# Performance work log

Measured on AMD Instinct MI355X. Metric: run time of the kernel, lower is better.

Reference implementation:

```python
import jax, jax.numpy as jnp
import numpy as np

N, D = 4096, 512
NUM_CLASSES = 100


def setup_inputs() -> dict:
    key = jax.random.key(0)
    k1, k2, k3 = jax.random.split(key, 3)
    image_features = jax.random.normal(k1, (N, D), dtype=jnp.float32)
    text_features = jax.random.normal(k2, (N, D), dtype=jnp.float32)
    labels = jax.random.randint(k3, (N,), 0, NUM_CLASSES, dtype=jnp.int64)
    return {
        "image_features": image_features,
        "text_features": text_features,
        "labels": labels,
    }


def reference(image_features, text_features, labels):
    # mask[i,j] = 1 if labels[i] != labels[j] else 0 (vectorized O(N^2) loops)
    mask = (labels[:, None] != labels[None, :]).astype(image_features.dtype)  # [N,N]

    # L2-normalize along feature dim (F.normalize, p=2, dim=1)
    img = image_features / jnp.linalg.norm(image_features, axis=1, keepdims=True)
    txt = text_features / jnp.linalg.norm(text_features, axis=1, keepdims=True)

    # neg_similarity = sum(exp((txt @ img.T) @ mask))  -- faithful to source
    sim = txt @ img.T                      # [N,N]
    neg_similarity = jnp.sum(jnp.exp(sim @ mask))

    # pos_sim_i = exp(<img_i, txt_i>); loss_i = log(pos / (pos + neg))
    pos_sim = jnp.exp(jnp.sum(img * txt, axis=1))  # [N]
    pos_log = jnp.log(pos_sim / (pos_sim + neg_similarity))
    return -jnp.sum(pos_log)
```

## Files before the change

kernel.cpp:

```cpp
#include <hip/hip_runtime.h>

#define NN 4096
#define DD 512
#define CP 128
#define MT 16
#define NBB 256
#define LROWS 64

#define NEG   0
#define DONE  1
#define D_OFF 16
#define CNTF_OFF (16 + NN)
#define GB_OFF_W (16 + NN + CP)

typedef __attribute__((ext_vector_type(8))) short bf16x8;
typedef __attribute__((ext_vector_type(4))) float f32x4;

static __device__ inline unsigned short f2bf(float f) {
    unsigned int u = __float_as_uint(f);
    unsigned int r = u + 0x7fffu + ((u >> 16) & 1u);
    return (unsigned short)(r >> 16);
}

__global__ __launch_bounds__(512, 1) void kA(const float* __restrict__ img,
                                             const int* __restrict__ labels,
                                             float* __restrict__ ws) {
    __shared__ __align__(16) float lrows[LROWS * DD];
    __shared__ int   wlist[8][32];
    __shared__ int   wcnt[8];
    __shared__ int   soff[9];
    __shared__ int   flat[256];
    __shared__ float sinv[256];
    int c = blockIdx.x, t = threadIdx.x, w = t >> 6, l = t & 63;

    if (c == 0 && t == 0) { ws[NEG] = 0.0f; ((int*)ws)[DONE] = 0; }

    int cnt = 0;
    for (int it = 0; it < 8; ++it) {
        int row = (w << 9) + (it << 6) + l;
        int lab = labels[row];
        unsigned long long m = __ballot(lab == c);
        if (lab == c) {
            int pos = cnt + (int)__popcll(m & ((1ull << l) - 1ull));
            if (pos < 32) wlist[w][pos] = row;
        }
        cnt += (int)__popcll(m);
    }
    if (l == 0) wcnt[w] = cnt < 32 ? cnt : 32;
    __syncthreads();
    if (t == 0) {
        int o = 0;
        #pragma unroll
        for (int i = 0; i < 8; ++i) { soff[i] = o; o += wcnt[i]; }
        soff[8] = o;
    }
    __syncthreads();
    int n = soff[8];
    for (int s = l; s < wcnt[w]; s += 64) flat[soff[w] + s] = wlist[w][s];
    __syncthreads();

    int nl = n < LROWS ? n : LROWS;
    const float4* img4 = (const float4*)img;
    float4* lr4 = (float4*)lrows;

    for (int idx = t; idx < nl * 128; idx += 512) {
        int r = idx >> 7, c4 = idx & 127;
        lr4[r * 128 + c4] = img4[(size_t)flat[r] * 128 + c4];
    }
    __syncthreads();

    for (int s = w; s < n; s += 8) {
        float4 v0, v1;
        if (s < nl) { v0 = lr4[s * 128 + l]; v1 = lr4[s * 128 + 64 + l]; }
        else { int j = flat[s]; v0 = img4[(size_t)j * 128 + l]; v1 = img4[(size_t)j * 128 + 64 + l]; }
        float ss = v0.x*v0.x + v0.y*v0.y + v0.z*v0.z + v0.w*v0.w
                 + v1.x*v1.x + v1.y*v1.y + v1.z*v1.z + v1.w*v1.w;
        #pragma unroll
        for (int o = 32; o >= 1; o >>= 1) ss += __shfl_xor(ss, o);
        if (l == 0) sinv[s] = rsqrtf(ss);
    }
    __syncthreads();

    float acc = 0.f;
    #pragma unroll 8
    for (int s = 0; s < nl; ++s) acc += lrows[s * DD + t] * sinv[s];
    for (int s = nl; s < n; ++s) acc += img[(size_t)flat[s] * DD + t] * sinv[s];

    unsigned short* gbf = (unsigned short*)(ws + GB_OFF_W);
    gbf[(size_t)c * DD + t] = f2bf(acc);
    if (t == 0) ws[CNTF_OFF + c] = (float)n;
}

__global__ __launch_bounds__(256, 1) void kB(const float* __restrict__ img,
                                             const float* __restrict__ txt,
                                             float* __restrict__ ws,
                                             float* __restrict__ out) {
    __shared__ __align__(16) unsigned char As[MT * 1024];
    __shared__ __align__(16) unsigned char Bs[CP * 1024];
    __shared__ float cnts[CP];
    __shared__ float part[4][MT];
    __shared__ float Ss[MT];
    __shared__ float wred[4];
    __shared__ float sneg;
    __shared__ int   sdone;

    int t = threadIdx.x, w = t >> 6, l = t & 63;
    int b = blockIdx.x;
    int row0 = b * MT;
    int* wsi = (int*)ws;

    #pragma unroll
    for (int i = 0; i < 4; ++i) {
        int lr  = w * 4 + i;
        int row = row0 + lr;
        const float4* i4 = (const float4*)(img + (size_t)row * DD);
        const float4* t4 = (const float4*)(txt + (size_t)row * DD);
        float4 a0 = i4[l], a1 = i4[l + 64];
        float4 b0 = t4[l], b1 = t4[l + 64];
        float ssi = a0.x*a0.x + a0.y*a0.y + a0.z*a0.z + a0.w*a0.w
                  + a1.x*a1.x + a1.y*a1.y + a1.z*a1.z + a1.w*a1.w;
        float sst = b0.x*b0.x + b0.y*b0.y + b0.z*b0.z + b0.w*b0.w
                  + b1.x*b1.x + b1.y*b1.y + b1.z*b1.z + b1.w*b1.w;
        float dot = a0.x*b0.x + a0.y*b0.y + a0.z*b0.z + a0.w*b0.w
                  + a1.x*b1.x + a1.y*b1.y + a1.z*b1.z + a1.w*b1.w;
        #pragma unroll
        for (int o = 32; o >= 1; o >>= 1) {
            ssi += __shfl_xor(ssi, o);
            sst += __shfl_xor(sst, o);
            dot += __shfl_xor(dot, o);
        }
        float inv_t = rsqrtf(sst);
        ushort4 s0, s1;
        s0.x = f2bf(b0.x*inv_t); s0.y = f2bf(b0.y*inv_t);
        s0.z = f2bf(b0.z*inv_t); s0.w = f2bf(b0.w*inv_t);
        s1.x = f2bf(b1.x*inv_t); s1.y = f2bf(b1.y*inv_t);
        s1.z = f2bf(b1.z*inv_t); s1.w = f2bf(b1.w*inv_t);
        int swz = (lr & 7) << 4;
        *(ushort4*)&As[lr * 1024 + ((8 * l) ^ swz)]       = s0;
        *(ushort4*)&As[lr * 1024 + 512 + ((8 * l) ^ swz)] = s1;
        if (l == 0) {
            float inv_i = rsqrtf(ssi);
            ws[D_OFF + row] = dot * inv_i * inv_t;
        }
    }
    if (t < CP) cnts[t] = ws[CNTF_OFF + t];

    {
        const int4* gB = (const int4*)(ws + GB_OFF_W);
        int co = t & 63;
        #pragma unroll 8
        for (int s = 0; s < 32; ++s) {
            int4 v = gB[s * 256 + t];
            int c = 4 * s + (t >> 6);
            *(int4*)&Bs[c * 1024 + ((co * 16) ^ ((c & 7) << 4))] = v;
        }
    }
    __syncthreads();

    f32x4 acc0 = {0.f,0.f,0.f,0.f}, acc1 = {0.f,0.f,0.f,0.f};
    int arow = l & 15, kq = l >> 4;
    int aswz = (arow & 7) << 4;
    int c0 = 32 * w;
    int cA = c0 + arow,    cB = cA + 16;
    int aoffA = cA * 1024, aswzA = (cA & 7) << 4;
    int aoffB = cB * 1024, aswzB = (cB & 7) << 4;
    #pragma unroll
    for (int ch = 0; ch < 16; ++ch) {
        int kb = ch * 64 + kq * 16;
        bf16x8 af = *(const bf16x8*)&As[arow * 1024 + (kb ^ aswz)];
        bf16x8 b0 = *(const bf16x8*)&Bs[aoffA + (kb ^ aswzA)];
        bf16x8 b1 = *(const bf16x8*)&Bs[aoffB + (kb ^ aswzB)];
        acc0 = __builtin_amdgcn_mfma_f32_16x16x32_bf16(af, b0, acc0, 0, 0, 0);
        acc1 = __builtin_amdgcn_mfma_f32_16x16x32_bf16(af, b1, acc1, 0, 0, 0);
    }

    float rsum[4];
    #pragma unroll
    for (int r = 0; r < 4; ++r) {
        float s = acc0[r] + acc1[r];
        #pragma unroll
        for (int o = 1; o < 16; o <<= 1) s += __shfl_xor(s, o);
        rsum[r] = s;
    }
    if ((l & 15) == 0) {
        #pragma unroll
        for (int r = 0; r < 4; ++r) part[w][kq * 4 + r] = rsum[r];
    }
    __syncthreads();
    if (t < MT) Ss[t] = part[0][t] + part[1][t] + part[2][t] + part[3][t];
    __syncthreads();
    float p;
    {
        float e0 = 0.f, e1 = 0.f;
        #pragma unroll
        for (int r = 0; r < 4; ++r) {
            e0 += __expf(Ss[kq * 4 + r] - acc0[r]);
            e1 += __expf(Ss[kq * 4 + r] - acc1[r]);
        }
        p = cnts[cA] * e0 + cnts[cB] * e1;
    }
    #pragma unroll
    for (int o = 32; o >= 1; o >>= 1) p += __shfl_xor(p, o);
    if (l == 0) wred[w] = p;
    __syncthreads();
    if (t == 0) {
        atomicAdd(ws + NEG, wred[0] + wred[1] + wred[2] + wred[3]);
        __threadfence();
        int old = atomicAdd(wsi + DONE, 1);
        sdone = (old == NBB - 1);
        if (sdone) sneg = atomicAdd(ws + NEG, 0.0f);
    }
    __syncthreads();
    if (sdone) {
        __threadfence();
        float neg = sneg;
        float s = 0.f;
        #pragma unroll 4
        for (int i = t; i < NN; i += 256) {
            float dv = ws[D_OFF + i];
            s += logf(__expf(dv) + neg) - dv;
        }
        #pragma unroll
        for (int o = 32; o >= 1; o >>= 1) s += __shfl_xor(s, o);
        __syncthreads();
        if (l == 0) wred[w] = s;
        __syncthreads();
        if (t == 0) out[0] = wred[0] + wred[1] + wred[2] + wred[3];
    }
}

extern "C" void kernel_launch(void* const* d_in, const int* in_sizes, int n_in,
                              void* d_out, int out_size, void* d_ws, size_t ws_size,
                              hipStream_t stream) {
    const float* img  = (const float*)d_in[0];
    const float* txt  = (const float*)d_in[1];
    const int* labels = (const int*)d_in[2];
    float* ws  = (float*)d_ws;
    float* out = (float*)d_out;

    kA<<<CP,  512, 0, stream>>>(img, labels, ws);
    kB<<<NBB, 256, 0, stream>>>(img, txt, ws, out);
}
```

Measured before the change: 94.37 us.

## Double kB threads to 512 and batch global loads into registers

Kernel kB moves from 4 to 8 waves per block, so each wave now owns 2 rows of the text tile and 16 class columns with a single MFMA accumulator. All global loads (img/txt rows and the bf16 class-sum matrix) are issued up front into registers before any compute or LDS stores, so more memory requests are in flight at once. The row copy into LDS in kA is likewise split into a batched load phase followed by a store phase. The cost is higher register pressure from the 16-element int4 and float4 staging arrays, and the block reductions now combine 8 wave partials.

```diff
diff --git a/kernel.cpp b/kernel.cpp
--- a/kernel.cpp
+++ b/kernel.cpp
@@ -63,9 +63,19 @@
     const float4* img4 = (const float4*)img;
     float4* lr4 = (float4*)lrows;
 
-    for (int idx = t; idx < nl * 128; idx += 512) {
-        int r = idx >> 7, c4 = idx & 127;
-        lr4[r * 128 + c4] = img4[(size_t)flat[r] * 128 + c4];
+    {
+        int total = nl * 128;
+        float4 tv[16];
+        #pragma unroll
+        for (int k = 0; k < 16; ++k) {
+            int idx = t + (k << 9);
+            if (idx < total) tv[k] = img4[(size_t)flat[idx >> 7] * 128 + (idx & 127)];
+        }
+        #pragma unroll
+        for (int k = 0; k < 16; ++k) {
+            int idx = t + (k << 9);
+            if (idx < total) lr4[idx] = tv[k];
+        }
     }
     __syncthreads();
 
@@ -91,16 +101,16 @@
     if (t == 0) ws[CNTF_OFF + c] = (float)n;
 }
 
-__global__ __launch_bounds__(256, 1) void kB(const float* __restrict__ img,
+__global__ __launch_bounds__(512, 1) void kB(const float* __restrict__ img,
                                              const float* __restrict__ txt,
                                              float* __restrict__ ws,
                                              float* __restrict__ out) {
     __shared__ __align__(16) unsigned char As[MT * 1024];
     __shared__ __align__(16) unsigned char Bs[CP * 1024];
     __shared__ float cnts[CP];
-    __shared__ float part[4][MT];
+    __shared__ float part[8][MT];
     __shared__ float Ss[MT];
-    __shared__ float wred[4];
+    __shared__ float wred[8];
     __shared__ float sneg;
     __shared__ int   sdone;
 
@@ -109,14 +119,26 @@
     int row0 = b * MT;
     int* wsi = (int*)ws;
 
-    #pragma unroll
-    for (int i = 0; i < 4; ++i) {
-        int lr  = w * 4 + i;
+    float4 iA0[2], iA1[2], tB0[2], tB1[2];
+    #pragma unroll
+    for (int i = 0; i < 2; ++i) {
+        int row = row0 + 2 * w + i;
+        const float4* i4  = (const float4*)(img + (size_t)row * DD);
+        const float4* t4p = (const float4*)(txt + (size_t)row * DD);
+        iA0[i] = i4[l];  iA1[i] = i4[l + 64];
+        tB0[i] = t4p[l]; tB1[i] = t4p[l + 64];
+    }
+    int4 gr[16];
+    const int4* gB = (const int4*)(ws + GB_OFF_W);
+    #pragma unroll
+    for (int s = 0; s < 16; ++s) gr[s] = gr[s] = gB[s * 512 + t];
+    if (t < CP) cnts[t] = ws[CNTF_OFF + t];
+
+    #pragma unroll
+    for (int i = 0; i < 2; ++i) {
+        int lr  = 2 * w + i;
         int row = row0 + lr;
-        const float4* i4 = (const float4*)(img + (size_t)row * DD);
-        const float4* t4 = (const float4*)(txt + (size_t)row * DD);
-        float4 a0 = i4[l], a1 = i4[l + 64];
-        float4 b0 = t4[l], b1 = t4[l + 64];
+        float4 a0 = iA0[i], a1 = iA1[i], b0 = tB0[i], b1 = tB1[i];
         float ssi = a0.x*a0.x + a0.y*a0.y + a0.z*a0.z + a0.w*a0.w
                   + a1.x*a1.x + a1.y*a1.y + a1.z*a1.z + a1.w*a1.w;
         float sst = b0.x*b0.x + b0.y*b0.y + b0.z*b0.z + b0.w*b0.w
@@ -143,41 +165,31 @@
             ws[D_OFF + row] = dot * inv_i * inv_t;
         }
     }
-    if (t < CP) cnts[t] = ws[CNTF_OFF + t];
-
-    {
-        const int4* gB = (const int4*)(ws + GB_OFF_W);
-        int co = t & 63;
-        #pragma unroll 8
-        for (int s = 0; s < 32; ++s) {
-            int4 v = gB[s * 256 + t];
-            int c = 4 * s + (t >> 6);
-            *(int4*)&Bs[c * 1024 + ((co * 16) ^ ((c & 7) << 4))] = v;
-        }
-    }
-    __syncthreads();
-
-    f32x4 acc0 = {0.f,0.f,0.f,0.f}, acc1 = {0.f,0.f,0.f,0.f};
+
+    #pragma unroll
+    for (int s = 0; s < 16; ++s) {
+        int c = 8 * s + w;
+        *(int4*)&Bs[c * 1024 + ((l * 16) ^ ((c & 7) << 4))] = gr[s];
+    }
+    __syncthreads();
+
+    f32x4 acc = {0.f, 0.f, 0.f, 0.f};
     int arow = l & 15, kq = l >> 4;
     int aswz = (arow & 7) << 4;
-    int c0 = 32 * w;
-    int cA = c0 + arow,    cB = cA + 16;
+    int cA = 16 * w + arow;
     int aoffA = cA * 1024, aswzA = (cA & 7) << 4;
-    int aoffB = cB * 1024, aswzB = (cB & 7) << 4;
     #pragma unroll
     for (int ch = 0; ch < 16; ++ch) {
         int kb = ch * 64 + kq * 16;
         bf16x8 af = *(const bf16x8*)&As[arow * 1024 + (kb ^ aswz)];
-        bf16x8 b0 = *(const bf16x8*)&Bs[aoffA + (kb ^ aswzA)];
-        bf16x8 b1 = *(const bf16x8*)&Bs[aoffB + (kb ^ aswzB)];
-        acc0 = __builtin_amdgcn_mfma_f32_16x16x32_bf16(af, b0, acc0, 0, 0, 0);
-        acc1 = __builtin_amdgcn_mfma_f32_16x16x32_bf16(af, b1, acc1, 0, 0, 0);
+        bf16x8 bf = *(const bf16x8*)&Bs[aoffA + (kb ^ aswzA)];
+        acc = __builtin_amdgcn_mfma_f32_16x16x32_bf16(af, bf, acc, 0, 0, 0);
     }
 
     float rsum[4];
     #pragma unroll
     for (int r = 0; r < 4; ++r) {
-        float s = acc0[r] + acc1[r];
+        float s = acc[r];
         #pragma unroll
         for (int o = 1; o < 16; o <<= 1) s += __shfl_xor(s, o);
         rsum[r] = s;
@@ -187,24 +199,29 @@
         for (int r = 0; r < 4; ++r) part[w][kq * 4 + r] = rsum[r];
     }
     __syncthreads();
-    if (t < MT) Ss[t] = part[0][t] + part[1][t] + part[2][t] + part[3][t];
+    if (t < MT) {
+        float ssum = 0.f;
+        #pragma unroll
+        for (int g = 0; g < 8; ++g) ssum += part[g][t];
+        Ss[t] = ssum;
+    }
     __syncthreads();
     float p;
     {
-        float e0 = 0.f, e1 = 0.f;
-        #pragma unroll
-        for (int r = 0; r < 4; ++r) {
-            e0 += __expf(Ss[kq * 4 + r] - acc0[r]);
-            e1 += __expf(Ss[kq * 4 + r] - acc1[r]);
-        }
-        p = cnts[cA] * e0 + cnts[cB] * e1;
+        float e0 = 0.f;
+        #pragma unroll
+        for (int r = 0; r < 4; ++r) e0 += __expf(Ss[kq * 4 + r] - acc[r]);
+        p = cnts[cA] * e0;
     }
     #pragma unroll
     for (int o = 32; o >= 1; o >>= 1) p += __shfl_xor(p, o);
     if (l == 0) wred[w] = p;
     __syncthreads();
     if (t == 0) {
-        atomicAdd(ws + NEG, wred[0] + wred[1] + wred[2] + wred[3]);
+        float ptot = 0.f;
+        #pragma unroll
+        for (int g = 0; g < 8; ++g) ptot += wred[g];
+        atomicAdd(ws + NEG, ptot);
         __threadfence();
         int old = atomicAdd(wsi + DONE, 1);
         sdone = (old == NBB - 1);
@@ -216,7 +233,7 @@
         float neg = sneg;
         float s = 0.f;
         #pragma unroll 4
-        for (int i = t; i < NN; i += 256) {
+        for (int i = t; i < NN; i += 512) {
             float dv = ws[D_OFF + i];
             s += logf(__expf(dv) + neg) - dv;
         }
@@ -225,7 +242,12 @@
         __syncthreads();
         if (l == 0) wred[w] = s;
         __syncthreads();
-        if (t == 0) out[0] = wred[0] + wred[1] + wred[2] + wred[3];
+        if (t == 0) {
+            float stot = 0.f;
+            #pragma unroll
+            for (int g = 0; g < 8; ++g) stot += wred[g];
+            out[0] = stot;
+        }
     }
 }
 
@@ -239,5 +261,5 @@
     float* out = (float*)d_out;
 
     kA<<<CP,  512, 0, stream>>>(img, labels, ws);
-    kB<<<NBB, 256, 0, stream>>>(img, txt, ws, out);
-}
+    kB<<<NBB, 512, 0, stream>>>(img, txt, ws, out);
+}
```

Result: slower. 110.0 us (+16.5%).
